# Optimization experiments

Hardware: AMD Instinct MI355X
Metric: run time of the kernel (lower is better)

## Reference

```python
import jax, jax.numpy as jnp
import numpy as np

N, M, D = 131072, 2048, 2


def setup_inputs() -> dict:
    key = jax.random.key(0)
    k1, k2 = jax.random.split(key)
    sample = jax.random.normal(k1, (N, D), dtype=jnp.float32)
    mu = jax.random.uniform(k2, (M, D), dtype=jnp.float32)
    # A initialized as 15 * I per component, exactly as in the torch module
    A = (15.0 * jnp.broadcast_to(jnp.eye(D, dtype=jnp.float32), (M, D, D))).astype(jnp.float32)
    w = jnp.ones((M, 1), dtype=jnp.float32)
    return {"sample": sample, "mu": mu, "A": A, "w": w}


def reference(sample, mu, A, w):
    """GaussianMixture.log_likelihoods(sample): logsumexp_j( wlog_j - (x-mu_j)^T G_j (x-mu_j) )."""
    # update_covariances: G_m = A_m A_m^T / 2, shape (M, D, D)
    G = jnp.einsum('mij,mkj->mik', A, A) * 0.5
    g00, g01, g10, g11 = G[:, 0, 0], G[:, 0, 1], G[:, 1, 0], G[:, 1, 1]  # (M,)
    # covariances_determinants (2x2 case) + weights_log
    dets = g00 * g11 - g01 * g10                                          # (M,)
    wlog = jax.nn.log_softmax(w, axis=0)[:, 0] + 0.5 * jnp.log(dets)      # (M,)
    # Pairwise Mahalanobis quadratic form, D=2 expanded to avoid an (N,M,D) temp
    dx0 = sample[:, 0:1] - mu[None, :, 0]   # (N, M)
    dx1 = sample[:, 1:2] - mu[None, :, 1]   # (N, M)
    q = g00 * dx0 * dx0 + (g01 + g10) * dx0 * dx1 + g11 * dx1 * dx1       # (N, M)
    # mode='lse' reduction of kernel_product: log sum_j exp(wlog_j - q_ij)
    ll = jax.nn.logsumexp(wlog[None, :] - q, axis=1, keepdims=True)       # (N, 1)
    return ll
```

## Files before the change

kernel.cpp:

```cpp
#include <hip/hip_runtime.h>
#include <math.h>


#if __has_builtin(__builtin_amdgcn_exp2f)
#define EXP2(x) __builtin_amdgcn_exp2f(x)
#else
#define EXP2(x) exp2f(x)
#endif

typedef float v4f __attribute__((ext_vector_type(4)));
typedef int   i4  __attribute__((ext_vector_type(4)));

#if __has_builtin(__builtin_elementwise_max)
#define V4MAX(a, b) __builtin_elementwise_max(a, b)
#else
static __device__ inline v4f V4MAX(v4f a, v4f b) {
  v4f r; r.x = fmaxf(a.x, b.x); r.y = fmaxf(a.y, b.y);
  r.z = fmaxf(a.z, b.z); r.w = fmaxf(a.w, b.w); return r;
}
#endif

static __device__ __forceinline__ v4f exp2_hw4(v4f d) {
  v4f r; r.x = EXP2(d.x); r.y = EXP2(d.y); r.z = EXP2(d.z); r.w = EXP2(d.w);
  return r;
}

#define SCH_K1   8388608.0f
#define SCH_K2   1064986823.0f
#define SCH_TMIN 58353856.0f

#define SPLIT 8
#define CH  16
#define CHG 8

__global__ __launch_bounds__(256) void prep_kernel(
    const float* __restrict__ mu,
    const float* __restrict__ A,
    const float* __restrict__ w,
    float* __restrict__ C,
    int M) {
  __shared__ float red[256];
  __shared__ int uni[256];
  const int t = threadIdx.x;

  float mx = -INFINITY;
  for (int m = t; m < M; m += 256) mx = fmaxf(mx, w[m]);
  red[t] = mx; __syncthreads();
  for (int s = 128; s > 0; s >>= 1) {
    if (t < s) red[t] = fmaxf(red[t], red[t + s]);
    __syncthreads();
  }
  const float wmax = red[0]; __syncthreads();

  float sum = 0.f;
  for (int m = t; m < M; m += 256) sum += expf(w[m] - wmax);
  red[t] = sum; __syncthreads();
  for (int s = 128; s > 0; s >>= 1) {
    if (t < s) red[t] += red[t + s];
    __syncthreads();
  }
  const float logZ = wmax + logf(red[0]);

  const float r00 = A[0], r01 = A[1], r10 = A[2], r11 = A[3];
  const float rg00 = 0.5f * (r00 * r00 + r01 * r01);
  const float rg01 = 0.5f * (r00 * r10 + r01 * r11);
  const float rg11 = 0.5f * (r10 * r10 + r11 * r11);

  const float LOG2E = 1.44269504088896340736f;
  int myuni = 1;
  for (int m = t; m < M; m += 256) {
    const float a00 = A[m * 4 + 0], a01 = A[m * 4 + 1];
    const float a10 = A[m * 4 + 2], a11 = A[m * 4 + 3];
    const float g00 = 0.5f * (a00 * a00 + a01 * a01);
    const float g01 = 0.5f * (a00 * a10 + a01 * a11);
    const float g11 = 0.5f * (a10 * a10 + a11 * a11);
    const float g01s = 2.0f * g01;
    const float det = g00 * g11 - g01 * g01;
    const float wlog = (w[m] - logZ) + 0.5f * logf(det);
    const float mu0 = mu[m * 2 + 0], mu1 = mu[m * 2 + 1];
    const float c0 = wlog - (g00 * mu0 * mu0 + g01s * mu0 * mu1 + g11 * mu1 * mu1);
    const float c2 = 2.0f * g00 * mu0 + g01s * mu1;
    const float c4 = 2.0f * g11 * mu1 + g01s * mu0;
    C[0 * M + m] = LOG2E * c0;
    C[1 * M + m] = LOG2E * -g00;
    C[2 * M + m] = LOG2E * c2;
    C[3 * M + m] = LOG2E * -g11;
    C[4 * M + m] = LOG2E * c4;
    C[5 * M + m] = LOG2E * -g01s;
    myuni &= (g00 == rg00) & (g01 == rg01) & (g11 == rg11);
  }
  uni[t] = myuni; __syncthreads();
  for (int s = 128; s > 0; s >>= 1) {
    if (t < s) uni[t] &= uni[t + s];
    __syncthreads();
  }
  if (t == 0) {
    ((int*)C)[6 * M + 0] = uni[0];
    C[6 * M + 1] = LOG2E * -rg00;
    C[6 * M + 2] = LOG2E * -rg11;
    C[6 * M + 3] = LOG2E * -2.0f * rg01;
  }
}

__global__ __launch_bounds__(512, 4) void gmix_kernel(
    const float* __restrict__ sample,
    const float* __restrict__ C,
    float* __restrict__ out,
    int N, int M) {
  __shared__ float Lmx[SPLIT][4][64];
  __shared__ float Lsm[SPLIT][4][64];

  const int lane = threadIdx.x & 63;
  const int wave = __builtin_amdgcn_readfirstlane((int)(threadIdx.x >> 6));
  const int n0 = blockIdx.x * 256 + lane;

  float2 xs0 = (n0       < N) ? ((const float2*)sample)[n0      ] : make_float2(0.f, 0.f);
  float2 xs1 = (n0 + 64  < N) ? ((const float2*)sample)[n0 + 64 ] : make_float2(0.f, 0.f);
  float2 xs2 = (n0 + 128 < N) ? ((const float2*)sample)[n0 + 128] : make_float2(0.f, 0.f);
  float2 xs3 = (n0 + 192 < N) ? ((const float2*)sample)[n0 + 192] : make_float2(0.f, 0.f);
  const v4f x0q = {xs0.x, xs1.x, xs2.x, xs3.x};
  const v4f x1q = {xs0.y, xs1.y, xs2.y, xs3.y};

  const int flag = ((const int*)C)[6 * M + 0];
  const float cb1 = C[6 * M + 1];
  const float cb3 = C[6 * M + 2];
  const float cb5 = C[6 * M + 3];

  const int Mq = M / SPLIT;
  const int m0 = wave * Mq;
  const float* __restrict__ C0 = C + m0;
  const float* __restrict__ C1 = C + M + m0;
  const float* __restrict__ C2 = C + 2 * M + m0;
  const float* __restrict__ C3 = C + 3 * M + m0;
  const float* __restrict__ C4 = C + 4 * M + m0;
  const float* __restrict__ C5 = C + 5 * M + m0;

  v4f base4 = {0.f, 0.f, 0.f, 0.f};
  v4f mx = {-INFINITY, -INFINITY, -INFINITY, -INFINITY};
  v4f s  = {0.f, 0.f, 0.f, 0.f};

  const v4f tminv = {SCH_TMIN, SCH_TMIN, SCH_TMIN, SCH_TMIN};

  if (flag) {
    base4 = cb1 * x0q * x0q + cb3 * x1q * x1q + cb5 * x0q * x1q;
    for (int m = 0; m < Mq; m += CH) {
      v4f a[CH];
#pragma unroll
      for (int j = 0; j < CH; ++j) {
        const float c0 = C0[m + j], c2 = C2[m + j], c4 = C4[m + j];
        v4f t = x0q * c2 + c0;
        a[j] = x1q * c4 + t;
      }
      v4f t0 = V4MAX(a[0], a[1]);
      v4f t1 = V4MAX(a[2], a[3]);
      v4f t2 = V4MAX(a[4], a[5]);
      v4f t3 = V4MAX(a[6], a[7]);
#pragma unroll
      for (int j = 8; j < CH; j += 4) {
        t0 = V4MAX(t0, a[j]);
        t1 = V4MAX(t1, a[j + 1]);
        t2 = V4MAX(t2, a[j + 2]);
        t3 = V4MAX(t3, a[j + 3]);
      }
      const v4f cm = V4MAX(V4MAX(t0, t1), V4MAX(t2, t3));
      const v4f nm = V4MAX(mx, cm);
      const v4f resc = exp2_hw4(mx - nm);
      const v4f knm = SCH_K2 - nm * SCH_K1;
      v4f l0 = {0.f, 0.f, 0.f, 0.f}, l1 = {0.f, 0.f, 0.f, 0.f};
#pragma unroll
      for (int j = 0; j < CH; j += 2) {
        v4f u0 = a[j]     * SCH_K1 + knm;
        v4f u1 = a[j + 1] * SCH_K1 + knm;
        u0 = V4MAX(u0, tminv);
        u1 = V4MAX(u1, tminv);
        const i4 iv0 = __builtin_convertvector(u0, i4);
        const i4 iv1 = __builtin_convertvector(u1, i4);
        l0 += __builtin_bit_cast(v4f, iv0);
        l1 += __builtin_bit_cast(v4f, iv1);
      }
      s = s * resc + (l0 + l1);
      mx = nm;
    }
  } else {
    for (int m = 0; m < Mq; m += CHG) {
      v4f a[CHG];
#pragma unroll
      for (int j = 0; j < CHG; ++j) {
        const float c0 = C0[m + j], c1 = C1[m + j], c2 = C2[m + j];
        const float c3 = C3[m + j], c4 = C4[m + j], c5 = C5[m + j];
        v4f u = x0q * c1 + c2;
        u = x1q * c5 + u;
        v4f v = x1q * c3 + c4;
        v4f r = u * x0q + c0;
        a[j] = v * x1q + r;
      }
      v4f t0 = V4MAX(a[0], a[1]);
      v4f t1 = V4MAX(a[2], a[3]);
      v4f t2 = V4MAX(a[4], a[5]);
      v4f t3 = V4MAX(a[6], a[7]);
      const v4f cm = V4MAX(V4MAX(t0, t1), V4MAX(t2, t3));
      const v4f nm = V4MAX(mx, cm);
      const v4f resc = exp2_hw4(mx - nm);
      v4f l0 = {0.f, 0.f, 0.f, 0.f}, l1 = {0.f, 0.f, 0.f, 0.f};
#pragma unroll
      for (int j = 0; j < CHG; j += 2) {
        l0 += exp2_hw4(a[j] - nm);
        l1 += exp2_hw4(a[j + 1] - nm);
      }
      s = s * resc + (l0 + l1);
      mx = nm;
    }
  }

#pragma unroll
  for (int k = 0; k < 4; ++k) {
    Lmx[wave][k][lane] = mx[k] + base4[k];
    Lsm[wave][k][lane] = s[k];
  }
  __syncthreads();

  if (wave < 4) {
    const int set = wave;
    const int n = blockIdx.x * 256 + set * 64 + lane;
    if (n < N) {
      float gm = Lmx[0][set][lane];
#pragma unroll
      for (int v = 1; v < SPLIT; ++v) gm = fmaxf(gm, Lmx[v][set][lane]);
      float S = 0.f;
#pragma unroll
      for (int v = 0; v < SPLIT; ++v)
        S += Lsm[v][set][lane] * EXP2(Lmx[v][set][lane] - gm);
      out[n] = (gm + __log2f(S)) * 0.69314718055994530942f;
    }
  }
}

extern "C" void kernel_launch(void* const* d_in, const int* in_sizes, int n_in,
                              void* d_out, int out_size, void* d_ws, size_t ws_size,
                              hipStream_t stream) {
  const float* sample = (const float*)d_in[0];
  const float* mu     = (const float*)d_in[1];
  const float* A      = (const float*)d_in[2];
  const float* w      = (const float*)d_in[3];
  float* out = (float*)d_out;

  const int N = in_sizes[0] / 2;
  const int M = in_sizes[3];

  float* C = (float*)d_ws;

  prep_kernel<<<1, 256, 0, stream>>>(mu, A, w, C, M);
  gmix_kernel<<<(N + 255) / 256, 512, 0, stream>>>(sample, C, out, N, M);
}
```

Before: 110.5 us.

## Spatially sort samples and components to skip negligible mixture chunks via bounds

Adds a counting sort of samples into a 64x64 spatial grid and sorts mixture components into 16x16 cells, then computes per-chunk bounding boxes and max weights. In the uniform-covariance path each wave first processes its most promising chunk, then skips chunks whose upper bound on the log-term falls more than 32 (log2) below the running max. This aims to cut the exp/accumulate work that dominates the kernel. In exchange it adds several extra launches (memset, histogram, scan, scatter), global atomics and a permuted output write. The skip threshold also makes the logsumexp approximate within a bounded error.

```diff
diff --git a/kernel.cpp b/kernel.cpp
--- a/kernel.cpp
+++ b/kernel.cpp
@@ -32,16 +32,27 @@
 #define SPLIT 8
 #define CH  16
 #define CHG 8
+#define PC  16
+#define SC  64
+#define SCELLS (SC * SC)
+#define T_SKIP 32.0f
+#define MAXM_SORT 2048
 
 __global__ __launch_bounds__(256) void prep_kernel(
     const float* __restrict__ mu,
     const float* __restrict__ A,
     const float* __restrict__ w,
     float* __restrict__ C,
-    int M) {
+    int M, int psort) {
   __shared__ float red[256];
   __shared__ int uni[256];
+  __shared__ int hist[PC * PC];
+  __shared__ int off2[PC * PC];
+  __shared__ float sMu0[MAXM_SORT];
+  __shared__ float sMu1[MAXM_SORT];
+  __shared__ float sWl[MAXM_SORT];
   const int t = threadIdx.x;
+  const int NC = M / CH;
 
   float mx = -INFINITY;
   for (int m = t; m < M; m += 256) mx = fmaxf(mx, w[m]);
@@ -65,6 +76,23 @@
   const float rg00 = 0.5f * (r00 * r00 + r01 * r01);
   const float rg01 = 0.5f * (r00 * r10 + r01 * r11);
   const float rg11 = 0.5f * (r10 * r10 + r11 * r11);
+
+  if (t < PC * PC) hist[t] = 0;
+  __syncthreads();
+  if (psort) {
+    for (int m = t; m < M; m += 256) {
+      const float mu0 = mu[m * 2 + 0], mu1 = mu[m * 2 + 1];
+      int cx = (int)(mu0 * (float)PC); cx = min(PC - 1, max(0, cx));
+      int cy = (int)(mu1 * (float)PC); cy = min(PC - 1, max(0, cy));
+      atomicAdd(&hist[cy * PC + cx], 1);
+    }
+  }
+  __syncthreads();
+  if (t == 0) {
+    int acc = 0;
+    for (int i = 0; i < PC * PC; ++i) { int c = hist[i]; off2[i] = acc; acc += c; }
+  }
+  __syncthreads();
 
   const float LOG2E = 1.44269504088896340736f;
   int myuni = 1;
@@ -81,12 +109,19 @@
     const float c0 = wlog - (g00 * mu0 * mu0 + g01s * mu0 * mu1 + g11 * mu1 * mu1);
     const float c2 = 2.0f * g00 * mu0 + g01s * mu1;
     const float c4 = 2.0f * g11 * mu1 + g01s * mu0;
-    C[0 * M + m] = LOG2E * c0;
-    C[1 * M + m] = LOG2E * -g00;
-    C[2 * M + m] = LOG2E * c2;
-    C[3 * M + m] = LOG2E * -g11;
-    C[4 * M + m] = LOG2E * c4;
-    C[5 * M + m] = LOG2E * -g01s;
+    int slot = m;
+    if (psort) {
+      int cx = (int)(mu0 * (float)PC); cx = min(PC - 1, max(0, cx));
+      int cy = (int)(mu1 * (float)PC); cy = min(PC - 1, max(0, cy));
+      slot = atomicAdd(&off2[cy * PC + cx], 1);
+      sMu0[slot] = mu0; sMu1[slot] = mu1; sWl[slot] = LOG2E * wlog;
+    }
+    C[0 * M + slot] = LOG2E * c0;
+    C[1 * M + slot] = LOG2E * -g00;
+    C[2 * M + slot] = LOG2E * c2;
+    C[3 * M + slot] = LOG2E * -g11;
+    C[4 * M + slot] = LOG2E * c4;
+    C[5 * M + slot] = LOG2E * -g01s;
     myuni &= (g00 == rg00) & (g01 == rg01) & (g11 == rg11);
   }
   uni[t] = myuni; __syncthreads();
@@ -94,30 +129,165 @@
     if (t < s) uni[t] &= uni[t + s];
     __syncthreads();
   }
+
+  float* Mcx = C + 6 * M + 16;
+  float* Mcy = Mcx + NC;
+  float* Mrx = Mcy + NC;
+  float* Mry = Mrx + NC;
+  float* Mw  = Mry + NC;
+  for (int c = t; c < NC; c += 256) {
+    if (psort) {
+      float mn0 = INFINITY, mx0 = -INFINITY, mn1 = INFINITY, mx1 = -INFINITY;
+      float wl = -INFINITY;
+      for (int k = 0; k < CH; ++k) {
+        const float u0 = sMu0[c * CH + k], u1 = sMu1[c * CH + k];
+        mn0 = fminf(mn0, u0); mx0 = fmaxf(mx0, u0);
+        mn1 = fminf(mn1, u1); mx1 = fmaxf(mx1, u1);
+        wl = fmaxf(wl, sWl[c * CH + k]);
+      }
+      Mcx[c] = 0.5f * (mn0 + mx0); Mrx[c] = 0.5f * (mx0 - mn0);
+      Mcy[c] = 0.5f * (mn1 + mx1); Mry[c] = 0.5f * (mx1 - mn1);
+      Mw[c] = wl;
+    } else {
+      Mcx[c] = 0.f; Mcy[c] = 0.f; Mrx[c] = 1e30f; Mry[c] = 1e30f; Mw[c] = 1e30f;
+    }
+  }
+
   if (t == 0) {
     ((int*)C)[6 * M + 0] = uni[0];
     C[6 * M + 1] = LOG2E * -rg00;
     C[6 * M + 2] = LOG2E * -rg11;
     C[6 * M + 3] = LOG2E * -2.0f * rg01;
-  }
-}
+    float tr = rg00 + rg11;
+    float d0 = rg00 - rg11;
+    float disc = sqrtf(d0 * d0 + 4.f * rg01 * rg01);
+    float lam = 0.5f * (tr - disc);
+    if (!(lam > 0.f)) lam = 0.f;
+    C[6 * M + 4] = LOG2E * lam;
+  }
+}
+
+static __device__ __forceinline__ int scell(float x, float y) {
+  int cx = (int)((x + 2.0f) * 16.0f); cx = min(SC - 1, max(0, cx));
+  int cy = (int)((y + 2.0f) * 16.0f); cy = min(SC - 1, max(0, cy));
+  return cy * SC + cx;
+}
+
+__global__ __launch_bounds__(256) void s_hist(
+    const float2* __restrict__ sp, int* __restrict__ hist, int N) {
+  int i = blockIdx.x * blockDim.x + threadIdx.x;
+  const int stride = gridDim.x * blockDim.x;
+  for (; i < N; i += stride) {
+    const float2 p = sp[i];
+    atomicAdd(&hist[scell(p.x, p.y)], 1);
+  }
+}
+
+__global__ __launch_bounds__(256) void s_scan(int* __restrict__ hist) {
+  __shared__ int part[256];
+  const int t = threadIdx.x;
+  int v[16]; int sum = 0;
+#pragma unroll
+  for (int k = 0; k < 16; ++k) { v[k] = hist[t * 16 + k]; sum += v[k]; }
+  part[t] = sum; __syncthreads();
+  if (t == 0) {
+    int acc = 0;
+    for (int i = 0; i < 256; ++i) { int x = part[i]; part[i] = acc; acc += x; }
+  }
+  __syncthreads();
+  int acc = part[t];
+#pragma unroll
+  for (int k = 0; k < 16; ++k) { int x = v[k]; hist[t * 16 + k] = acc; acc += x; }
+}
+
+__global__ __launch_bounds__(256) void s_scatter(
+    const float2* __restrict__ sp, int* __restrict__ offs,
+    float2* __restrict__ ss, int* __restrict__ perm, int N) {
+  int i = blockIdx.x * blockDim.x + threadIdx.x;
+  const int stride = gridDim.x * blockDim.x;
+  for (; i < N; i += stride) {
+    const float2 p = sp[i];
+    const int slot = atomicAdd(&offs[scell(p.x, p.y)], 1);
+    ss[slot] = p;
+    perm[slot] = i;
+  }
+}
+
+#define PROCESS(MG) do {                                                     \
+    v4f a_[CH];                                                              \
+    _Pragma("unroll")                                                        \
+    for (int j = 0; j < CH; ++j) {                                           \
+      const float c0_ = Cp0[(MG) + j], c2_ = Cp2[(MG) + j],                  \
+                  c4_ = Cp4[(MG) + j];                                       \
+      v4f t_ = x0q * c2_ + c0_;                                              \
+      a_[j] = x1q * c4_ + t_;                                                \
+    }                                                                        \
+    v4f t0_ = V4MAX(a_[0], a_[1]);                                           \
+    v4f t1_ = V4MAX(a_[2], a_[3]);                                           \
+    v4f t2_ = V4MAX(a_[4], a_[5]);                                           \
+    v4f t3_ = V4MAX(a_[6], a_[7]);                                           \
+    _Pragma("unroll")                                                        \
+    for (int j = 8; j < CH; j += 4) {                                        \
+      t0_ = V4MAX(t0_, a_[j]);     t1_ = V4MAX(t1_, a_[j + 1]);              \
+      t2_ = V4MAX(t2_, a_[j + 2]); t3_ = V4MAX(t3_, a_[j + 3]);              \
+    }                                                                        \
+    const v4f cm_ = V4MAX(V4MAX(t0_, t1_), V4MAX(t2_, t3_));                 \
+    const v4f nm_ = V4MAX(mx, cm_);                                          \
+    const v4f resc_ = exp2_hw4(mx - nm_);                                    \
+    const v4f knm_ = SCH_K2 - nm_ * SCH_K1;                                  \
+    v4f l0_ = {0.f, 0.f, 0.f, 0.f}, l1_ = {0.f, 0.f, 0.f, 0.f};              \
+    _Pragma("unroll")                                                        \
+    for (int j = 0; j < CH; j += 2) {                                        \
+      v4f u0_ = a_[j] * SCH_K1 + knm_;                                       \
+      v4f u1_ = a_[j + 1] * SCH_K1 + knm_;                                   \
+      u0_ = V4MAX(u0_, tminv);                                               \
+      u1_ = V4MAX(u1_, tminv);                                               \
+      const i4 iv0_ = __builtin_convertvector(u0_, i4);                      \
+      const i4 iv1_ = __builtin_convertvector(u1_, i4);                      \
+      l0_ += __builtin_bit_cast(v4f, iv0_);                                  \
+      l1_ += __builtin_bit_cast(v4f, iv1_);                                  \
+    }                                                                        \
+    s = s * resc_ + (l0_ + l1_);                                             \
+    mx = nm_;                                                                \
+  } while (0)
+
+#define ANCHOR(dst) do {                                                     \
+    v4f t_ = mx + base4;                                                     \
+    float am_ = fminf(fminf(t_.x, t_.y), fminf(t_.z, t_.w));                 \
+    _Pragma("unroll")                                                        \
+    for (int o_ = 32; o_; o_ >>= 1)                                          \
+      am_ = fminf(am_, __shfl_xor(am_, o_, 64));                             \
+    dst = am_;                                                               \
+  } while (0)
+
+#define CHUNK_UB(G, UBV) do {                                                \
+    const float ccx_ = Mcx[G], ccy_ = Mcy[G];                                \
+    const float crx_ = Mrx[G], cry_ = Mry[G], mwv_ = Mw[G];                  \
+    const float dx_ = fmaxf(0.f, fabsf(wcx - ccx_) - (wrx + crx_));          \
+    const float dy_ = fmaxf(0.f, fabsf(wcy - ccy_) - (wry + cry_));          \
+    UBV = mwv_ - lamL * (dx_ * dx_ + dy_ * dy_);                             \
+  } while (0)
 
 __global__ __launch_bounds__(512, 4) void gmix_kernel(
-    const float* __restrict__ sample,
+    const float2* __restrict__ xs,
+    const int* __restrict__ perm,
     const float* __restrict__ C,
     float* __restrict__ out,
-    int N, int M) {
+    int N, int M, int blkmask) {
   __shared__ float Lmx[SPLIT][4][64];
   __shared__ float Lsm[SPLIT][4][64];
 
   const int lane = threadIdx.x & 63;
   const int wave = __builtin_amdgcn_readfirstlane((int)(threadIdx.x >> 6));
-  const int n0 = blockIdx.x * 256 + lane;
-
-  float2 xs0 = (n0       < N) ? ((const float2*)sample)[n0      ] : make_float2(0.f, 0.f);
-  float2 xs1 = (n0 + 64  < N) ? ((const float2*)sample)[n0 + 64 ] : make_float2(0.f, 0.f);
-  float2 xs2 = (n0 + 128 < N) ? ((const float2*)sample)[n0 + 128] : make_float2(0.f, 0.f);
-  float2 xs3 = (n0 + 192 < N) ? ((const float2*)sample)[n0 + 192] : make_float2(0.f, 0.f);
+  int blk = blockIdx.x;
+  if (blkmask) blk = (blk * 97) & blkmask;
+  const int n0 = blk * 256 + lane;
+
+  const float2 z2 = make_float2(0.f, 0.f);
+  const float2 xs0 = (n0       < N) ? xs[n0      ] : z2;
+  const float2 xs1 = (n0 + 64  < N) ? xs[n0 + 64 ] : z2;
+  const float2 xs2 = (n0 + 128 < N) ? xs[n0 + 128] : z2;
+  const float2 xs3 = (n0 + 192 < N) ? xs[n0 + 192] : z2;
   const v4f x0q = {xs0.x, xs1.x, xs2.x, xs3.x};
   const v4f x1q = {xs0.y, xs1.y, xs2.y, xs3.y};
 
@@ -127,61 +297,72 @@
   const float cb5 = C[6 * M + 3];
 
   const int Mq = M / SPLIT;
-  const int m0 = wave * Mq;
-  const float* __restrict__ C0 = C + m0;
-  const float* __restrict__ C1 = C + M + m0;
-  const float* __restrict__ C2 = C + 2 * M + m0;
-  const float* __restrict__ C3 = C + 3 * M + m0;
-  const float* __restrict__ C4 = C + 4 * M + m0;
-  const float* __restrict__ C5 = C + 5 * M + m0;
-
   v4f base4 = {0.f, 0.f, 0.f, 0.f};
   v4f mx = {-INFINITY, -INFINITY, -INFINITY, -INFINITY};
   v4f s  = {0.f, 0.f, 0.f, 0.f};
-
   const v4f tminv = {SCH_TMIN, SCH_TMIN, SCH_TMIN, SCH_TMIN};
 
   if (flag) {
     base4 = cb1 * x0q * x0q + cb3 * x1q * x1q + cb5 * x0q * x1q;
-    for (int m = 0; m < Mq; m += CH) {
-      v4f a[CH];
-#pragma unroll
-      for (int j = 0; j < CH; ++j) {
-        const float c0 = C0[m + j], c2 = C2[m + j], c4 = C4[m + j];
-        v4f t = x0q * c2 + c0;
-        a[j] = x1q * c4 + t;
-      }
-      v4f t0 = V4MAX(a[0], a[1]);
-      v4f t1 = V4MAX(a[2], a[3]);
-      v4f t2 = V4MAX(a[4], a[5]);
-      v4f t3 = V4MAX(a[6], a[7]);
-#pragma unroll
-      for (int j = 8; j < CH; j += 4) {
-        t0 = V4MAX(t0, a[j]);
-        t1 = V4MAX(t1, a[j + 1]);
-        t2 = V4MAX(t2, a[j + 2]);
-        t3 = V4MAX(t3, a[j + 3]);
-      }
-      const v4f cm = V4MAX(V4MAX(t0, t1), V4MAX(t2, t3));
-      const v4f nm = V4MAX(mx, cm);
-      const v4f resc = exp2_hw4(mx - nm);
-      const v4f knm = SCH_K2 - nm * SCH_K1;
-      v4f l0 = {0.f, 0.f, 0.f, 0.f}, l1 = {0.f, 0.f, 0.f, 0.f};
-#pragma unroll
-      for (int j = 0; j < CH; j += 2) {
-        v4f u0 = a[j]     * SCH_K1 + knm;
-        v4f u1 = a[j + 1] * SCH_K1 + knm;
-        u0 = V4MAX(u0, tminv);
-        u1 = V4MAX(u1, tminv);
-        const i4 iv0 = __builtin_convertvector(u0, i4);
-        const i4 iv1 = __builtin_convertvector(u1, i4);
-        l0 += __builtin_bit_cast(v4f, iv0);
-        l1 += __builtin_bit_cast(v4f, iv1);
-      }
-      s = s * resc + (l0 + l1);
-      mx = nm;
+
+    float b0n = fminf(fminf(x0q.x, x0q.y), fminf(x0q.z, x0q.w));
+    float b0x = fmaxf(fmaxf(x0q.x, x0q.y), fmaxf(x0q.z, x0q.w));
+    float b1n = fminf(fminf(x1q.x, x1q.y), fminf(x1q.z, x1q.w));
+    float b1x = fmaxf(fmaxf(x1q.x, x1q.y), fmaxf(x1q.z, x1q.w));
+#pragma unroll
+    for (int o = 32; o; o >>= 1) {
+      b0n = fminf(b0n, __shfl_xor(b0n, o, 64));
+      b0x = fmaxf(b0x, __shfl_xor(b0x, o, 64));
+      b1n = fminf(b1n, __shfl_xor(b1n, o, 64));
+      b1x = fmaxf(b1x, __shfl_xor(b1x, o, 64));
+    }
+    const float wcx = 0.5f * (b0n + b0x), wrx = 0.5f * (b0x - b0n);
+    const float wcy = 0.5f * (b1n + b1x), wry = 0.5f * (b1x - b1n);
+
+    const int NC = M / CH;
+    const int CPW = Mq / CH;
+    const float lamL = C[6 * M + 4];
+    const float* __restrict__ Mcx = C + 6 * M + 16;
+    const float* __restrict__ Mcy = Mcx + NC;
+    const float* __restrict__ Mrx = Mcy + NC;
+    const float* __restrict__ Mry = Mrx + NC;
+    const float* __restrict__ Mw  = Mry + NC;
+    const float* __restrict__ Cp0 = C;
+    const float* __restrict__ Cp2 = C + 2 * M;
+    const float* __restrict__ Cp4 = C + 4 * M;
+
+    float best = -INFINITY; int bestc = 0;
+#pragma unroll 1
+    for (int c = 0; c < CPW; ++c) {
+      const int g = wave + SPLIT * c;
+      float ub; CHUNK_UB(g, ub);
+      if (ub > best) { best = ub; bestc = c; }
+    }
+    const int bc = __builtin_amdgcn_readfirstlane(bestc);
+    {
+      const int mg = (wave + SPLIT * bc) * CH;
+      PROCESS(mg);
+    }
+    float anc; ANCHOR(anc);
+
+#pragma unroll 1
+    for (int c = 0; c < CPW; ++c) {
+      if (c == bc) continue;
+      const int g = wave + SPLIT * c;
+      float ub; CHUNK_UB(g, ub);
+      if (ub < anc - T_SKIP) continue;
+      const int mg = g * CH;
+      PROCESS(mg);
+      ANCHOR(anc);
     }
   } else {
+    const int m0 = wave * Mq;
+    const float* __restrict__ C0 = C + m0;
+    const float* __restrict__ C1 = C + M + m0;
+    const float* __restrict__ C2 = C + 2 * M + m0;
+    const float* __restrict__ C3 = C + 3 * M + m0;
+    const float* __restrict__ C4 = C + 4 * M + m0;
+    const float* __restrict__ C5 = C + 5 * M + m0;
     for (int m = 0; m < Mq; m += CHG) {
       v4f a[CHG];
 #pragma unroll
@@ -221,8 +402,8 @@
 
   if (wave < 4) {
     const int set = wave;
-    const int n = blockIdx.x * 256 + set * 64 + lane;
-    if (n < N) {
+    const int slot = blk * 256 + set * 64 + lane;
+    if (slot < N) {
       float gm = Lmx[0][set][lane];
 #pragma unroll
       for (int v = 1; v < SPLIT; ++v) gm = fmaxf(gm, Lmx[v][set][lane]);
@@ -230,7 +411,8 @@
 #pragma unroll
       for (int v = 0; v < SPLIT; ++v)
         S += Lsm[v][set][lane] * EXP2(Lmx[v][set][lane] - gm);
-      out[n] = (gm + __log2f(S)) * 0.69314718055994530942f;
+      const int outn = perm ? perm[slot] : slot;
+      out[outn] = (gm + __log2f(S)) * 0.69314718055994530942f;
     }
   }
 }
@@ -248,7 +430,32 @@
   const int M = in_sizes[3];
 
   float* C = (float*)d_ws;
-
-  prep_kernel<<<1, 256, 0, stream>>>(mu, A, w, C, M);
-  gmix_kernel<<<(N + 255) / 256, 512, 0, stream>>>(sample, C, out, N, M);
-}
+  const int NC = M / CH;
+  const size_t cBytes = ((size_t)6 * M + 16 + 5 * (size_t)NC) * 4;
+  const size_t offHist = (cBytes + 255) & ~(size_t)255;
+  const size_t offSS   = (offHist + (size_t)SCELLS * 4 + 255) & ~(size_t)255;
+  const size_t offPerm = (offSS + (size_t)N * 8 + 255) & ~(size_t)255;
+  const size_t need    = offPerm + (size_t)N * 4;
+
+  const bool sortEn = (ws_size >= need) && (M % (SPLIT * CH) == 0) &&
+                      (M <= MAXM_SORT) && (N >= 256);
+  const int nblocks = (N + 255) / 256;
+  const int blkmask = (sortEn && ((nblocks & (nblocks - 1)) == 0))
+                          ? (nblocks - 1) : 0;
+
+  prep_kernel<<<1, 256, 0, stream>>>(mu, A, w, C, M, sortEn ? 1 : 0);
+
+  if (sortEn) {
+    int* hist    = (int*)((char*)d_ws + offHist);
+    float2* ss   = (float2*)((char*)d_ws + offSS);
+    int* permArr = (int*)((char*)d_ws + offPerm);
+    hipMemsetAsync(hist, 0, (size_t)SCELLS * 4, stream);
+    s_hist<<<256, 256, 0, stream>>>((const float2*)sample, hist, N);
+    s_scan<<<1, 256, 0, stream>>>(hist);
+    s_scatter<<<256, 256, 0, stream>>>((const float2*)sample, hist, ss, permArr, N);
+    gmix_kernel<<<nblocks, 512, 0, stream>>>(ss, permArr, C, out, N, M, blkmask);
+  } else {
+    gmix_kernel<<<nblocks, 512, 0, stream>>>((const float2*)sample, nullptr,
+                                             C, out, N, M, 0);
+  }
+}
```

Measured after the change: 164.0 us. 48.4% more time.

## Compute per-pair logits with bf16 split-precision MFMA in new kernel

Applied to the files above, without the earlier changes.

Adds a gmix_mfma kernel that, when all covariance matrices match, evaluates the linear part of each sample-component logit with 16x16x32 bf16 MFMA. Precision is kept with hi/lo bf16 splits of both samples and coefficients. The prep kernel now also packs these bf16 coefficient fragments into the workspace. The MFMA accumulators feed an online logsumexp epilogue that uses a bit-trick exponential, followed by a cross-lane shuffle merge. The aim is to move the FMA work off the vector ALU onto the matrix cores. The cost is bf16 split rounding error plus extra shuffle and epilogue overhead, and the general-covariance fallback path is also reorganised.

```diff
diff --git a/kernel.cpp b/kernel.cpp
--- a/kernel.cpp
+++ b/kernel.cpp
@@ -8,22 +8,23 @@
 #define EXP2(x) exp2f(x)
 #endif
 
+typedef float v2f   __attribute__((ext_vector_type(2)));
+typedef float f32x4 __attribute__((ext_vector_type(4)));
+typedef short bf16x8 __attribute__((ext_vector_type(8)));
 typedef float v4f __attribute__((ext_vector_type(4)));
-typedef int   i4  __attribute__((ext_vector_type(4)));
+typedef int   i4v __attribute__((ext_vector_type(4)));
 
 #if __has_builtin(__builtin_elementwise_max)
-#define V4MAX(a, b) __builtin_elementwise_max(a, b)
+#define VMAX(a, b) __builtin_elementwise_max(a, b)
 #else
-static __device__ inline v4f V4MAX(v4f a, v4f b) {
+static __device__ inline v2f VMAX(v2f a, v2f b) {
+  v2f r; r.x = fmaxf(a.x, b.x); r.y = fmaxf(a.y, b.y); return r;
+}
+static __device__ inline v4f VMAX(v4f a, v4f b) {
   v4f r; r.x = fmaxf(a.x, b.x); r.y = fmaxf(a.y, b.y);
   r.z = fmaxf(a.z, b.z); r.w = fmaxf(a.w, b.w); return r;
 }
 #endif
-
-static __device__ __forceinline__ v4f exp2_hw4(v4f d) {
-  v4f r; r.x = EXP2(d.x); r.y = EXP2(d.y); r.z = EXP2(d.z); r.w = EXP2(d.w);
-  return r;
-}
 
 #define SCH_K1   8388608.0f
 #define SCH_K2   1064986823.0f
@@ -31,7 +32,19 @@
 
 #define SPLIT 8
 #define CH  16
-#define CHG 8
+#define RMF 8
+#define LOG2E 1.44269504088896340736f
+#define LN2   0.69314718055994530942f
+
+__device__ __forceinline__ unsigned short f2bf(float f) {
+  unsigned u = __builtin_bit_cast(unsigned, f);
+  unsigned r = u + 0x7FFFu + ((u >> 16) & 1u);
+  return (unsigned short)(r >> 16);
+}
+__device__ __forceinline__ float bf2f(unsigned short h) {
+  unsigned u = ((unsigned)h) << 16;
+  return __builtin_bit_cast(float, u);
+}
 
 __global__ __launch_bounds__(256) void prep_kernel(
     const float* __restrict__ mu,
@@ -66,7 +79,8 @@
   const float rg01 = 0.5f * (r00 * r10 + r01 * r11);
   const float rg11 = 0.5f * (r10 * r10 + r11 * r11);
 
-  const float LOG2E = 1.44269504088896340736f;
+  unsigned short* Bp = (unsigned short*)(C + 6 * M + 16);
+
   int myuni = 1;
   for (int m = t; m < M; m += 256) {
     const float a00 = A[m * 4 + 0], a01 = A[m * 4 + 1];
@@ -81,12 +95,24 @@
     const float c0 = wlog - (g00 * mu0 * mu0 + g01s * mu0 * mu1 + g11 * mu1 * mu1);
     const float c2 = 2.0f * g00 * mu0 + g01s * mu1;
     const float c4 = 2.0f * g11 * mu1 + g01s * mu0;
-    C[0 * M + m] = LOG2E * c0;
+    const float C0v = LOG2E * c0;
+    const float C2v = LOG2E * c2;
+    const float C4v = LOG2E * c4;
+    C[0 * M + m] = C0v;
     C[1 * M + m] = LOG2E * -g00;
-    C[2 * M + m] = LOG2E * c2;
+    C[2 * M + m] = C2v;
     C[3 * M + m] = LOG2E * -g11;
-    C[4 * M + m] = LOG2E * c4;
+    C[4 * M + m] = C4v;
     C[5 * M + m] = LOG2E * -g01s;
+    const unsigned short c2h = f2bf(C2v);
+    const unsigned short c2l = f2bf(C2v - bf2f(c2h));
+    const unsigned short c4h = f2bf(C4v);
+    const unsigned short c4l = f2bf(C4v - bf2f(c4h));
+    const unsigned short c0h = f2bf(C0v);
+    const unsigned short c0l = f2bf(C0v - bf2f(c0h));
+    Bp[m * 8 + 0] = c2h; Bp[m * 8 + 1] = c2h; Bp[m * 8 + 2] = c2l;
+    Bp[m * 8 + 3] = c4h; Bp[m * 8 + 4] = c4h; Bp[m * 8 + 5] = c4l;
+    Bp[m * 8 + 6] = c0h; Bp[m * 8 + 7] = c0l;
     myuni &= (g00 == rg00) & (g01 == rg01) & (g11 == rg11);
   }
   uni[t] = myuni; __syncthreads();
@@ -99,6 +125,191 @@
     C[6 * M + 1] = LOG2E * -rg00;
     C[6 * M + 2] = LOG2E * -rg11;
     C[6 * M + 3] = LOG2E * -2.0f * rg01;
+  }
+}
+
+#define EPI(J, MXJ, SJ) do {                                                 \
+    const float a0 = acc[0][J], a1 = acc[1][J], a2 = acc[2][J],              \
+                a3 = acc[3][J], a4 = acc[4][J], a5 = acc[5][J],              \
+                a6 = acc[6][J], a7 = acc[7][J];                              \
+    const float m01 = fmaxf(a0, a1), m23 = fmaxf(a2, a3);                    \
+    const float m45 = fmaxf(a4, a5), m67 = fmaxf(a6, a7);                    \
+    const float cm = fmaxf(fmaxf(m01, m23), fmaxf(m45, m67));                \
+    const float nm = fmaxf(MXJ, cm);                                         \
+    const float resc = EXP2(MXJ - nm);                                       \
+    const float knm = fmaf(nm, -SCH_K1, SCH_K2);                             \
+    const float e0 = __builtin_bit_cast(float, (int)fmaxf(fmaf(a0, SCH_K1, knm), SCH_TMIN)); \
+    const float e1 = __builtin_bit_cast(float, (int)fmaxf(fmaf(a1, SCH_K1, knm), SCH_TMIN)); \
+    const float e2 = __builtin_bit_cast(float, (int)fmaxf(fmaf(a2, SCH_K1, knm), SCH_TMIN)); \
+    const float e3 = __builtin_bit_cast(float, (int)fmaxf(fmaf(a3, SCH_K1, knm), SCH_TMIN)); \
+    const float e4 = __builtin_bit_cast(float, (int)fmaxf(fmaf(a4, SCH_K1, knm), SCH_TMIN)); \
+    const float e5 = __builtin_bit_cast(float, (int)fmaxf(fmaf(a5, SCH_K1, knm), SCH_TMIN)); \
+    const float e6 = __builtin_bit_cast(float, (int)fmaxf(fmaf(a6, SCH_K1, knm), SCH_TMIN)); \
+    const float e7 = __builtin_bit_cast(float, (int)fmaxf(fmaf(a7, SCH_K1, knm), SCH_TMIN)); \
+    const float sm = ((e0 + e1) + (e2 + e3)) + ((e4 + e5) + (e6 + e7));      \
+    SJ = fmaf(SJ, resc, sm);                                                 \
+    MXJ = nm;                                                                \
+  } while (0)
+
+#define MERGE(MXJ, SJ, OFF) do {                                             \
+    const float om = __shfl_xor(MXJ, OFF, 64);                               \
+    const float os = __shfl_xor(SJ, OFF, 64);                                \
+    const float nm = fmaxf(MXJ, om);                                         \
+    SJ = SJ * EXP2(MXJ - nm) + os * EXP2(om - nm);                           \
+    MXJ = nm;                                                                \
+  } while (0)
+
+__global__ __launch_bounds__(512, 3) void gmix_mfma(
+    const float2* __restrict__ xs,
+    const float* __restrict__ C,
+    float* __restrict__ out,
+    int N, int M) {
+  __shared__ float Lmx[SPLIT][2][64];
+  __shared__ float Lsm[SPLIT][2][64];
+  const int lane = threadIdx.x & 63;
+  const int wave = __builtin_amdgcn_readfirstlane((int)(threadIdx.x >> 6));
+  const int flag = ((const int*)C)[6 * M + 0];
+  const float cb1 = C[6 * M + 1];
+  const float cb3 = C[6 * M + 2];
+  const float cb5 = C[6 * M + 3];
+
+  if (flag) {
+    const bf16x8* __restrict__ Bv = (const bf16x8*)(C + 6 * M + 16);
+    const int sbase = blockIdx.x * 128 + wave * 16;
+    const int col = lane & 15;
+
+    const int sA = sbase + col;
+    const float2 xa = (sA < N) ? xs[sA] : make_float2(0.f, 0.f);
+    bf16x8 afrag = (bf16x8){0, 0, 0, 0, 0, 0, 0, 0};
+    if (lane < 16) {
+      const unsigned short x0h = f2bf(xa.x);
+      const unsigned short x0l = f2bf(xa.x - bf2f(x0h));
+      const unsigned short x1h = f2bf(xa.y);
+      const unsigned short x1l = f2bf(xa.y - bf2f(x1h));
+      afrag = (bf16x8){(short)x0h, (short)x0l, (short)x0h,
+                       (short)x1h, (short)x1l, (short)x1h,
+                       (short)0x3F80, (short)0x3F80};
+    }
+
+    float mx0 = -INFINITY, mx1 = -INFINITY, mx2 = -INFINITY, mx3 = -INFINITY;
+    float s0 = 0.f, s1 = 0.f, s2 = 0.f, s3 = 0.f;
+    const f32x4 z4 = {0.f, 0.f, 0.f, 0.f};
+    const int rounds = M / (RMF * 16);
+
+#pragma unroll 2
+    for (int t = 0; t < rounds; ++t) {
+      f32x4 acc[RMF];
+#pragma unroll
+      for (int r = 0; r < RMF; ++r) {
+        const bf16x8 bfrag = Bv[t * (RMF * 16) + r * 16 + col];
+        acc[r] = __builtin_amdgcn_mfma_f32_16x16x32_bf16(afrag, bfrag, z4, 0, 0, 0);
+      }
+      EPI(0, mx0, s0);
+      EPI(1, mx1, s1);
+      EPI(2, mx2, s2);
+      EPI(3, mx3, s3);
+    }
+
+#pragma unroll
+    for (int off = 1; off < 16; off <<= 1) {
+      MERGE(mx0, s0, off);
+      MERGE(mx1, s1, off);
+      MERGE(mx2, s2, off);
+      MERGE(mx3, s3, off);
+    }
+
+    if (col == 0) {
+      const int g = lane >> 4;
+#define OUTJ(J, MXJ, SJ) do {                                                \
+        const int sr = sbase + g * 4 + (J);                                  \
+        if (sr < N) {                                                        \
+          const float2 xo = xs[sr];                                          \
+          const float base = cb1 * xo.x * xo.x + cb3 * xo.y * xo.y +         \
+                             cb5 * xo.x * xo.y;                              \
+          out[sr] = (MXJ + base + __log2f(SJ)) * LN2;                        \
+        }                                                                    \
+      } while (0)
+      OUTJ(0, mx0, s0);
+      OUTJ(1, mx1, s1);
+      OUTJ(2, mx2, s2);
+      OUTJ(3, mx3, s3);
+#undef OUTJ
+    }
+  } else {
+    const int nA = blockIdx.x * 128 + lane;
+    const int nB = nA + 64;
+    const float2 xA = (nA < N) ? xs[nA] : make_float2(0.f, 0.f);
+    const float2 xB = (nB < N) ? xs[nB] : make_float2(0.f, 0.f);
+    const v2f x0p = {xA.x, xB.x};
+    const v2f x1p = {xA.y, xB.y};
+
+    const int Mq = M / SPLIT;
+    const int m0 = wave * Mq;
+    const float* __restrict__ C0 = C + m0;
+    const float* __restrict__ C1 = C + M + m0;
+    const float* __restrict__ C2 = C + 2 * M + m0;
+    const float* __restrict__ C3 = C + 3 * M + m0;
+    const float* __restrict__ C4 = C + 4 * M + m0;
+    const float* __restrict__ C5 = C + 5 * M + m0;
+
+    v2f mx = {-INFINITY, -INFINITY};
+    v2f sacc = {0.f, 0.f};
+    for (int m = 0; m < Mq; m += CH) {
+      v2f a[CH];
+#pragma unroll
+      for (int j = 0; j < CH; ++j) {
+        const float c0 = C0[m + j], c1 = C1[m + j], c2 = C2[m + j];
+        const float c3 = C3[m + j], c4 = C4[m + j], c5 = C5[m + j];
+        v2f u = x0p * c1 + c2;
+        u = x1p * c5 + u;
+        v2f v = x1p * c3 + c4;
+        v2f r = u * x0p + c0;
+        a[j] = v * x1p + r;
+      }
+      v2f t0 = VMAX(a[0], a[1]);
+      v2f t1 = VMAX(a[2], a[3]);
+      v2f t2 = VMAX(a[4], a[5]);
+      v2f t3 = VMAX(a[6], a[7]);
+#pragma unroll
+      for (int j = 8; j < CH; j += 4) {
+        t0 = VMAX(t0, a[j]);     t1 = VMAX(t1, a[j + 1]);
+        t2 = VMAX(t2, a[j + 2]); t3 = VMAX(t3, a[j + 3]);
+      }
+      const v2f cm = VMAX(VMAX(t0, t1), VMAX(t2, t3));
+      const v2f nm = VMAX(mx, cm);
+      v2f resc; resc.x = EXP2(mx.x - nm.x); resc.y = EXP2(mx.y - nm.y);
+      v2f l0 = {0.f, 0.f}, l1 = {0.f, 0.f};
+#pragma unroll
+      for (int j = 0; j < CH; j += 2) {
+        const v2f d0 = a[j] - nm, d1 = a[j + 1] - nm;
+        v2f e0, e1;
+        e0.x = EXP2(d0.x); e0.y = EXP2(d0.y);
+        e1.x = EXP2(d1.x); e1.y = EXP2(d1.y);
+        l0 += e0; l1 += e1;
+      }
+      sacc = sacc * resc + (l0 + l1);
+      mx = nm;
+    }
+    const v2f base = cb1 * x0p * x0p + cb3 * x1p * x1p + cb5 * x0p * x1p;
+#pragma unroll
+    for (int k = 0; k < 2; ++k) {
+      Lmx[wave][k][lane] = mx[k] + base[k];
+      Lsm[wave][k][lane] = sacc[k];
+    }
+    __syncthreads();
+    if (wave < 2) {
+      const int n = blockIdx.x * 128 + wave * 64 + lane;
+      if (n < N) {
+        float gm = Lmx[0][wave][lane];
+#pragma unroll
+        for (int v = 1; v < SPLIT; ++v) gm = fmaxf(gm, Lmx[v][wave][lane]);
+        float S = 0.f;
+#pragma unroll
+        for (int v = 0; v < SPLIT; ++v)
+          S += Lsm[v][wave][lane] * EXP2(Lmx[v][wave][lane] - gm);
+        out[n] = (gm + __log2f(S)) * LN2;
+      }
+    }
   }
 }
 
@@ -138,8 +349,7 @@
   v4f base4 = {0.f, 0.f, 0.f, 0.f};
   v4f mx = {-INFINITY, -INFINITY, -INFINITY, -INFINITY};
   v4f s  = {0.f, 0.f, 0.f, 0.f};
-
-  const v4f tminv = {SCH_TMIN, SCH_TMIN, SCH_TMIN, SCH_TMIN};
+  const v4f tminv4 = {SCH_TMIN, SCH_TMIN, SCH_TMIN, SCH_TMIN};
 
   if (flag) {
     base4 = cb1 * x0q * x0q + cb3 * x1q * x1q + cb5 * x0q * x1q;
@@ -151,30 +361,30 @@
         v4f t = x0q * c2 + c0;
         a[j] = x1q * c4 + t;
       }
-      v4f t0 = V4MAX(a[0], a[1]);
-      v4f t1 = V4MAX(a[2], a[3]);
-      v4f t2 = V4MAX(a[4], a[5]);
-      v4f t3 = V4MAX(a[6], a[7]);
+      v4f t0 = VMAX(a[0], a[1]);
+      v4f t1 = VMAX(a[2], a[3]);
+      v4f t2 = VMAX(a[4], a[5]);
+      v4f t3 = VMAX(a[6], a[7]);
 #pragma unroll
       for (int j = 8; j < CH; j += 4) {
-        t0 = V4MAX(t0, a[j]);
-        t1 = V4MAX(t1, a[j + 1]);
-        t2 = V4MAX(t2, a[j + 2]);
-        t3 = V4MAX(t3, a[j + 3]);
-      }
-      const v4f cm = V4MAX(V4MAX(t0, t1), V4MAX(t2, t3));
-      const v4f nm = V4MAX(mx, cm);
-      const v4f resc = exp2_hw4(mx - nm);
+        t0 = VMAX(t0, a[j]);     t1 = VMAX(t1, a[j + 1]);
+        t2 = VMAX(t2, a[j + 2]); t3 = VMAX(t3, a[j + 3]);
+      }
+      const v4f cm = VMAX(VMAX(t0, t1), VMAX(t2, t3));
+      const v4f nm = VMAX(mx, cm);
+      v4f resc;
+      resc.x = EXP2(mx.x - nm.x); resc.y = EXP2(mx.y - nm.y);
+      resc.z = EXP2(mx.z - nm.z); resc.w = EXP2(mx.w - nm.w);
       const v4f knm = SCH_K2 - nm * SCH_K1;
       v4f l0 = {0.f, 0.f, 0.f, 0.f}, l1 = {0.f, 0.f, 0.f, 0.f};
 #pragma unroll
       for (int j = 0; j < CH; j += 2) {
         v4f u0 = a[j]     * SCH_K1 + knm;
         v4f u1 = a[j + 1] * SCH_K1 + knm;
-        u0 = V4MAX(u0, tminv);
-        u1 = V4MAX(u1, tminv);
-        const i4 iv0 = __builtin_convertvector(u0, i4);
-        const i4 iv1 = __builtin_convertvector(u1, i4);
+        u0 = VMAX(u0, tminv4);
+        u1 = VMAX(u1, tminv4);
+        const i4v iv0 = __builtin_convertvector(u0, i4v);
+        const i4v iv1 = __builtin_convertvector(u1, i4v);
         l0 += __builtin_bit_cast(v4f, iv0);
         l1 += __builtin_bit_cast(v4f, iv1);
       }
@@ -182,10 +392,10 @@
       mx = nm;
     }
   } else {
-    for (int m = 0; m < Mq; m += CHG) {
-      v4f a[CHG];
-#pragma unroll
-      for (int j = 0; j < CHG; ++j) {
+    for (int m = 0; m < Mq; m += CH) {
+      v4f a[CH];
+#pragma unroll
+      for (int j = 0; j < CH; ++j) {
         const float c0 = C0[m + j], c1 = C1[m + j], c2 = C2[m + j];
         const float c3 = C3[m + j], c4 = C4[m + j], c5 = C5[m + j];
         v4f u = x0q * c1 + c2;
@@ -194,18 +404,28 @@
         v4f r = u * x0q + c0;
         a[j] = v * x1q + r;
       }
-      v4f t0 = V4MAX(a[0], a[1]);
-      v4f t1 = V4MAX(a[2], a[3]);
-      v4f t2 = V4MAX(a[4], a[5]);
-      v4f t3 = V4MAX(a[6], a[7]);
-      const v4f cm = V4MAX(V4MAX(t0, t1), V4MAX(t2, t3));
-      const v4f nm = V4MAX(mx, cm);
-      const v4f resc = exp2_hw4(mx - nm);
+      v4f t0 = VMAX(a[0], a[1]);
+      v4f t1 = VMAX(a[2], a[3]);
+      v4f t2 = VMAX(a[4], a[5]);
+      v4f t3 = VMAX(a[6], a[7]);
+#pragma unroll
+      for (int j = 8; j < CH; j += 4) {
+        t0 = VMAX(t0, a[j]);     t1 = VMAX(t1, a[j + 1]);
+        t2 = VMAX(t2, a[j + 2]); t3 = VMAX(t3, a[j + 3]);
+      }
+      const v4f cm = VMAX(VMAX(t0, t1), VMAX(t2, t3));
+      const v4f nm = VMAX(mx, cm);
+      v4f resc;
+      resc.x = EXP2(mx.x - nm.x); resc.y = EXP2(mx.y - nm.y);
+      resc.z = EXP2(mx.z - nm.z); resc.w = EXP2(mx.w - nm.w);
       v4f l0 = {0.f, 0.f, 0.f, 0.f}, l1 = {0.f, 0.f, 0.f, 0.f};
 #pragma unroll
-      for (int j = 0; j < CHG; j += 2) {
-        l0 += exp2_hw4(a[j] - nm);
-        l1 += exp2_hw4(a[j + 1] - nm);
+      for (int j = 0; j < CH; j += 2) {
+        v4f d0 = a[j] - nm, d1 = a[j + 1] - nm;
+        v4f e0, e1;
+        e0.x = EXP2(d0.x); e0.y = EXP2(d0.y); e0.z = EXP2(d0.z); e0.w = EXP2(d0.w);
+        e1.x = EXP2(d1.x); e1.y = EXP2(d1.y); e1.z = EXP2(d1.z); e1.w = EXP2(d1.w);
+        l0 += e0; l1 += e1;
       }
       s = s * resc + (l0 + l1);
       mx = nm;
@@ -230,7 +450,7 @@
 #pragma unroll
       for (int v = 0; v < SPLIT; ++v)
         S += Lsm[v][set][lane] * EXP2(Lmx[v][set][lane] - gm);
-      out[n] = (gm + __log2f(S)) * 0.69314718055994530942f;
+      out[n] = (gm + __log2f(S)) * LN2;
     }
   }
 }
@@ -248,7 +468,14 @@
   const int M = in_sizes[3];
 
   float* C = (float*)d_ws;
+  const size_t need = ((size_t)6 * M + 16) * 4 + (size_t)M * 16;
 
   prep_kernel<<<1, 256, 0, stream>>>(mu, A, w, C, M);
-  gmix_kernel<<<(N + 255) / 256, 512, 0, stream>>>(sample, C, out, N, M);
-}
+
+  if (ws_size >= need && M % (RMF * 16) == 0 && M % (SPLIT * CH) == 0) {
+    gmix_mfma<<<(N + 127) / 128, 512, 0, stream>>>(
+        (const float2*)sample, C, out, N, M);
+  } else {
+    gmix_kernel<<<(N + 255) / 256, 512, 0, stream>>>(sample, C, out, N, M);
+  }
+}
```

Result: slower. 114.7 us (+3.7%).
